# Kernel optimization log

Hardware: AMD Instinct MI355X
Metric: run time of the kernel (lower is better)

The kernel has to match this reference:

```python
import jax, jax.numpy as jnp
import numpy as np

N = 100000      # nodes
E = 1600000     # edges (avg degree 16)
D_IN = 64
D_OUT = 64
EPS = 1e-9


def setup_inputs() -> dict:
    key = jax.random.key(0)
    ks = jax.random.split(key, 12)
    x = jax.random.normal(ks[0], (N, D_IN), dtype=jnp.float32)
    edge_row = jax.random.randint(ks[1], (E,), 0, N, dtype=jnp.int32)
    edge_col = jax.random.randint(ks[2], (E,), 0, N, dtype=jnp.int32)
    # positive normalized adjacency values (~1/degree scale)
    edge_val = jax.random.uniform(ks[3], (E,), dtype=jnp.float32) / 16.0
    lim = float(np.sqrt(6.0 / (D_IN + D_OUT)))  # xavier_uniform
    W0 = jax.random.uniform(ks[4], (D_OUT, D_IN), jnp.float32, -lim, lim)
    W1 = jax.random.uniform(ks[5], (D_OUT, D_IN), jnp.float32, -lim, lim)
    b0 = jnp.zeros((D_OUT,), jnp.float32)
    b1 = jnp.zeros((D_OUT,), jnp.float32)
    scale0 = jnp.ones((D_OUT,), jnp.float32)
    scale1 = jnp.ones((D_OUT,), jnp.float32)
    offset0 = jnp.zeros((D_OUT,), jnp.float32)
    offset1 = jnp.zeros((D_OUT,), jnp.float32)
    return {"x": x, "edge_val": edge_val, "W0": W0, "b0": b0,
            "scale0": scale0, "offset0": offset0, "W1": W1, "b1": b1,
            "scale1": scale1, "offset1": offset1,
            "edge_row": edge_row, "edge_col": edge_col}


def _hop_transform(feat, W, b, scale, offset):
    # Linear (no bias in nn.Linear) + separate bias + ReLU
    h = jax.nn.relu(feat @ W.T + b)                      # [N, D_OUT]
    # custom per-row normalization ('norm' branch)
    mean = jnp.mean(h, axis=1, keepdims=True)
    var = jnp.var(h, axis=1, keepdims=True) + EPS        # unbiased=False
    return (h - mean) * scale * jax.lax.rsqrt(var) + offset


def reference(x, edge_val, W0, b0, scale0, offset0, W1, b1, scale1, offset1,
              edge_row, edge_col):
    # SpMM: out[r] = sum_{e: row[e]==r} val[e] * x[col[e]]
    msgs = edge_val[:, None] * x[edge_col]               # [E, D_IN]
    agg = jax.ops.segment_sum(msgs, edge_row, num_segments=N)
    # order=1: hop-0 uses raw features, hop-1 uses aggregated features
    h0 = _hop_transform(x, W0, b0, scale0, offset0)
    h1 = _hop_transform(agg, W1, b1, scale1, offset1)
    # aggr='mean' -> elementwise sum of partial features
    return h0 + h1
```

## Files before the change

### kernel.cpp

```cpp
#include <hip/hip_runtime.h>

#define NN 100000
#define NE 1600000
#define DD 64
#define P    1563
#define NB   196
#define NBK1 391
#define BCAP 10240
#define PCAP 1536
#define ECAP 1536

__device__ __forceinline__ unsigned short f2bfu(float f) {
    union { float f; unsigned u; } c; c.f = f;
    unsigned lsb = (c.u >> 16) & 1u;
    c.u += 0x7FFFu + lsb;
    return (unsigned short)(c.u >> 16);
}

typedef short v8s __attribute__((ext_vector_type(8)));
typedef float v4f __attribute__((ext_vector_type(4)));

__global__ __launch_bounds__(256) void init_kernel(
    const float* __restrict__ W0, const float* __restrict__ W1,
    int* __restrict__ gbcur,
    unsigned short* __restrict__ wb0, unsigned short* __restrict__ wb1)
{
    int i = blockIdx.x * 256 + threadIdx.x;
    if (i < NB) gbcur[i] = 0;
    if (i < DD * DD) { wb0[i] = f2bfu(W0[i]); wb1[i] = f2bfu(W1[i]); }
}

__global__ __launch_bounds__(256) void bucket_scatter_kernel(
    const int* __restrict__ row, const int* __restrict__ col,
    const float* __restrict__ val, int* __restrict__ gbcur,
    int2* __restrict__ bslab)
{
    __shared__ int hist[NB];
    int b = blockIdx.x, t = threadIdx.x;
    if (t < NB) hist[t] = 0;
    __syncthreads();

    int4 r[4], c[4]; float4 v[4]; bool ok[4];
#pragma unroll
    for (int h = 0; h < 4; ++h) {
        int e = b * 4096 + h * 1024 + t * 4;
        ok[h] = (e + 3 < NE);
        if (ok[h]) {
            r[h] = *(const int4*)(row + e);
            c[h] = *(const int4*)(col + e);
            v[h] = *(const float4*)(val + e);
            atomicAdd(&hist[r[h].x >> 9], 1);
            atomicAdd(&hist[r[h].y >> 9], 1);
            atomicAdd(&hist[r[h].z >> 9], 1);
            atomicAdd(&hist[r[h].w >> 9], 1);
        }
    }
    __syncthreads();
    if (t < NB) {
        int cnt = hist[t];
        hist[t] = cnt ? atomicAdd(&gbcur[t], cnt) : 0;
    }
    __syncthreads();
#pragma unroll
    for (int h = 0; h < 4; ++h) {
        if (ok[h]) {
            int b0_ = r[h].x >> 9, b1_ = r[h].y >> 9;
            int b2_ = r[h].z >> 9, b3_ = r[h].w >> 9;
            int q0 = atomicAdd(&hist[b0_], 1);
            int q1 = atomicAdd(&hist[b1_], 1);
            int q2 = atomicAdd(&hist[b2_], 1);
            int q3 = atomicAdd(&hist[b3_], 1);
            if (q0 < BCAP) bslab[(size_t)b0_ * BCAP + q0] =
                make_int2(c[h].x | ((r[h].x & 511) << 20), __float_as_int(v[h].x));
            if (q1 < BCAP) bslab[(size_t)b1_ * BCAP + q1] =
                make_int2(c[h].y | ((r[h].y & 511) << 20), __float_as_int(v[h].y));
            if (q2 < BCAP) bslab[(size_t)b2_ * BCAP + q2] =
                make_int2(c[h].z | ((r[h].z & 511) << 20), __float_as_int(v[h].z));
            if (q3 < BCAP) bslab[(size_t)b3_ * BCAP + q3] =
                make_int2(c[h].w | ((r[h].w & 511) << 20), __float_as_int(v[h].w));
        }
    }
}

__global__ __launch_bounds__(256) void fine_scatter_kernel(
    const int* __restrict__ gbcur, const int2* __restrict__ bslab,
    int2* __restrict__ fslab, int* __restrict__ fcnt)
{
    __shared__ int cur[8];
    int b = blockIdx.x, t = threadIdx.x;
    int nb = min(gbcur[b], BCAP);
    const int2* bp = bslab + (size_t)b * BCAP;
    if (t < 8) cur[t] = 0;
    __syncthreads();
    for (int i = t; i < nb; i += 256) {
        int2 rc = bp[i];
        int rl = (rc.x >> 20) & 511;
        int lp = rl >> 6;
        int pos = atomicAdd(&cur[lp], 1);
        if (pos < PCAP)
            fslab[(size_t)(b * 8 + lp) * PCAP + pos] =
                make_int2((rc.x & 0x1FFFF) | ((rl & 63) << 20), rc.y);
    }
    __syncthreads();
    if (t < 8) fcnt[b * 8 + t] = min(cur[t], PCAP);
}

__global__ __launch_bounds__(256, 7) void sort_pull_mfma_kernel(
    const float* __restrict__ x, const int* __restrict__ fcnt,
    const int2* __restrict__ fslab,
    const unsigned short* __restrict__ wb0, const unsigned short* __restrict__ wb1,
    const float* __restrict__ b0, const float* __restrict__ s0, const float* __restrict__ o0,
    const float* __restrict__ b1, const float* __restrict__ s1, const float* __restrict__ o1,
    float* __restrict__ out)
{
    __shared__ int2 ebuf[ECAP];
    __shared__ unsigned aggt[4][16][36];
    __shared__ int rcnt[64];
    __shared__ int pscan[64];
    __shared__ int rcur[64];
    __shared__ int pstart[65];

    int p = blockIdx.x, t = threadIdx.x;
    int np = fcnt[p];
    const int2* sp = fslab + (size_t)p * PCAP;

    int2 rec[6]; int nrec = 0;
    if (t < 64) rcnt[t] = 0;
    __syncthreads();
#pragma unroll
    for (int k = 0; k < 6; ++k) {
        int i = t + k * 256;
        if (i < np) {
            rec[k] = sp[i]; ++nrec;
            atomicAdd(&rcnt[(rec[k].x >> 20) & 63], 1);
        }
    }
    __syncthreads();
    if (t < 64) pscan[t] = (rcnt[t] + 7) & ~7;
    __syncthreads();
    for (int off = 1; off < 64; off <<= 1) {
        int u = 0;
        if (t < 64 && t >= off) u = pscan[t - off];
        __syncthreads();
        if (t < 64) pscan[t] += u;
        __syncthreads();
    }
    if (t < 64) pstart[t + 1] = min(pscan[t], ECAP);
    if (t == 0) pstart[0] = 0;
    __syncthreads();
    if (t < 64) {
        rcur[t] = pstart[t];
        int s = min(pstart[t] + rcnt[t], ECAP);
        int e = pstart[t + 1];
        for (int j = s; j < e; ++j) ebuf[j] = make_int2(0, 0);
    }
    __syncthreads();
#pragma unroll
    for (int k = 0; k < 6; ++k) {
        if (k < nrec) {
            int pos = atomicAdd(&rcur[(rec[k].x >> 20) & 63], 1);
            if (pos < ECAP) ebuf[pos] = make_int2(rec[k].x & 0x1FFFF, rec[k].y);
        }
    }
    __syncthreads();

    int lane = t & 63, wv = t >> 6;
    int sub = lane & 15, q = lane >> 4;
    for (int rr = 0; rr < 16; ++rr) {
        int r = wv * 16 + rr;
        int start = pstart[r];
        int cc = (pstart[r + 1] - start) >> 3;
        float4 acc = make_float4(0.f, 0.f, 0.f, 0.f);
        int ch = 0;
        for (; ch + 2 <= cc; ch += 2) {
            int2 r0 = ebuf[start + ch * 8 + q];
            int2 r1 = ebuf[start + ch * 8 + 4 + q];
            int2 r2 = ebuf[start + ch * 8 + 8 + q];
            int2 r3 = ebuf[start + ch * 8 + 12 + q];
            float4 f0 = *(const float4*)(x + (size_t)r0.x * DD + sub * 4);
            float4 f1 = *(const float4*)(x + (size_t)r1.x * DD + sub * 4);
            float4 f2 = *(const float4*)(x + (size_t)r2.x * DD + sub * 4);
            float4 f3 = *(const float4*)(x + (size_t)r3.x * DD + sub * 4);
            float v0 = __int_as_float(r0.y), v1 = __int_as_float(r1.y);
            float v2 = __int_as_float(r2.y), v3 = __int_as_float(r3.y);
            acc.x = fmaf(v0, f0.x, acc.x); acc.y = fmaf(v0, f0.y, acc.y);
            acc.z = fmaf(v0, f0.z, acc.z); acc.w = fmaf(v0, f0.w, acc.w);
            acc.x = fmaf(v1, f1.x, acc.x); acc.y = fmaf(v1, f1.y, acc.y);
            acc.z = fmaf(v1, f1.z, acc.z); acc.w = fmaf(v1, f1.w, acc.w);
            acc.x = fmaf(v2, f2.x, acc.x); acc.y = fmaf(v2, f2.y, acc.y);
            acc.z = fmaf(v2, f2.z, acc.z); acc.w = fmaf(v2, f2.w, acc.w);
            acc.x = fmaf(v3, f3.x, acc.x); acc.y = fmaf(v3, f3.y, acc.y);
            acc.z = fmaf(v3, f3.z, acc.z); acc.w = fmaf(v3, f3.w, acc.w);
        }
        if (ch < cc) {
            int2 r0 = ebuf[start + ch * 8 + q];
            int2 r1 = ebuf[start + ch * 8 + 4 + q];
            float4 f0 = *(const float4*)(x + (size_t)r0.x * DD + sub * 4);
            float4 f1 = *(const float4*)(x + (size_t)r1.x * DD + sub * 4);
            float v0 = __int_as_float(r0.y), v1 = __int_as_float(r1.y);
            acc.x = fmaf(v0, f0.x, acc.x); acc.y = fmaf(v0, f0.y, acc.y);
            acc.z = fmaf(v0, f0.z, acc.z); acc.w = fmaf(v0, f0.w, acc.w);
            acc.x = fmaf(v1, f1.x, acc.x); acc.y = fmaf(v1, f1.y, acc.y);
            acc.z = fmaf(v1, f1.z, acc.z); acc.w = fmaf(v1, f1.w, acc.w);
        }
        acc.x += __shfl_xor(acc.x, 16, 64); acc.y += __shfl_xor(acc.y, 16, 64);
        acc.z += __shfl_xor(acc.z, 16, 64); acc.w += __shfl_xor(acc.w, 16, 64);
        acc.x += __shfl_xor(acc.x, 32, 64); acc.y += __shfl_xor(acc.y, 32, 64);
        acc.z += __shfl_xor(acc.z, 32, 64); acc.w += __shfl_xor(acc.w, 32, 64);
        if (q == 0) {
            uint2 pk;
            pk.x = (unsigned)f2bfu(acc.x) | ((unsigned)f2bfu(acc.y) << 16);
            pk.y = (unsigned)f2bfu(acc.z) | ((unsigned)f2bfu(acc.w) << 16);
            *(uint2*)&aggt[wv][rr][sub * 2] = pk;
        }
    }

    int nb0 = p * 64 + wv * 16;
    if (nb0 >= NN) return;

    v8s ax[2], aa[2];
#pragma unroll
    for (int ks = 0; ks < 2; ++ks) {
        const float* px = x + (size_t)(nb0 + sub) * DD + ks * 32 + q * 8;
        float4 a0 = *(const float4*)px, a1 = *(const float4*)(px + 4);
        v8s w;
        w[0] = (short)f2bfu(a0.x); w[1] = (short)f2bfu(a0.y);
        w[2] = (short)f2bfu(a0.z); w[3] = (short)f2bfu(a0.w);
        w[4] = (short)f2bfu(a1.x); w[5] = (short)f2bfu(a1.y);
        w[6] = (short)f2bfu(a1.z); w[7] = (short)f2bfu(a1.w);
        ax[ks] = w;
        aa[ks] = *(const v8s*)&aggt[wv][sub][ks * 16 + q * 4];
    }

    float h0v[4][4], h1v[4][4];
    float sr0[4] = {0,0,0,0}, sq0[4] = {0,0,0,0};
    float sr1[4] = {0,0,0,0}, sq1[4] = {0,0,0,0};
#pragma unroll
    for (int dt = 0; dt < 4; ++dt) {
        int nidx = dt * 16 + sub;
        float bi0 = b0[nidx], bi1 = b1[nidx];
        v8s w00 = *(const v8s*)(wb0 + nidx * 64 + q * 8);
        v8s w01 = *(const v8s*)(wb0 + nidx * 64 + 32 + q * 8);
        v8s w10 = *(const v8s*)(wb1 + nidx * 64 + q * 8);
        v8s w11 = *(const v8s*)(wb1 + nidx * 64 + 32 + q * 8);
        v4f c0 = (v4f){bi0, bi0, bi0, bi0};
        v4f c1 = (v4f){bi1, bi1, bi1, bi1};
        c0 = __builtin_amdgcn_mfma_f32_16x16x32_bf16(ax[0], w00, c0, 0, 0, 0);
        c0 = __builtin_amdgcn_mfma_f32_16x16x32_bf16(ax[1], w01, c0, 0, 0, 0);
        c1 = __builtin_amdgcn_mfma_f32_16x16x32_bf16(aa[0], w10, c1, 0, 0, 0);
        c1 = __builtin_amdgcn_mfma_f32_16x16x32_bf16(aa[1], w11, c1, 0, 0, 0);
#pragma unroll
        for (int r = 0; r < 4; ++r) {
            float h = fmaxf(c0[r], 0.f); h0v[dt][r] = h; sr0[r] += h; sq0[r] += h * h;
            float g = fmaxf(c1[r], 0.f); h1v[dt][r] = g; sr1[r] += g; sq1[r] += g * g;
        }
    }
#pragma unroll
    for (int off = 1; off < 16; off <<= 1) {
#pragma unroll
        for (int r = 0; r < 4; ++r) {
            sr0[r] += __shfl_xor(sr0[r], off, 64);
            sq0[r] += __shfl_xor(sq0[r], off, 64);
            sr1[r] += __shfl_xor(sr1[r], off, 64);
            sq1[r] += __shfl_xor(sq1[r], off, 64);
        }
    }

    float scl0[4], scl1[4], ofs0[4], ofs1[4];
#pragma unroll
    for (int dt = 0; dt < 4; ++dt) {
        int nidx = dt * 16 + sub;
        scl0[dt] = s0[nidx]; scl1[dt] = s1[nidx];
        ofs0[dt] = o0[nidx]; ofs1[dt] = o1[nidx];
    }

    const float inv = 1.0f / 64.0f;
#pragma unroll
    for (int r = 0; r < 4; ++r) {
        float m0 = sr0[r] * inv;
        float v0 = fmaxf(sq0[r] * inv - m0 * m0, 0.f) + 1e-9f;
        float m1 = sr1[r] * inv;
        float v1 = fmaxf(sq1[r] * inv - m1 * m1, 0.f) + 1e-9f;
        float rs0 = rsqrtf(v0), rs1 = rsqrtf(v1);
        int node = nb0 + q * 4 + r;
#pragma unroll
        for (int dt = 0; dt < 4; ++dt) {
            float rv = (h0v[dt][r] - m0) * scl0[dt] * rs0 + ofs0[dt]
                     + (h1v[dt][r] - m1) * scl1[dt] * rs1 + ofs1[dt];
            out[(size_t)node * DD + dt * 16 + sub] = rv;
        }
    }
}

extern "C" void kernel_launch(void* const* d_in, const int* in_sizes, int n_in,
                              void* d_out, int out_size, void* d_ws, size_t ws_size,
                              hipStream_t stream) {
    const float* x  = (const float*)d_in[0];
    const float* ev = (const float*)d_in[1];
    const float* W0 = (const float*)d_in[2];
    const float* b0 = (const float*)d_in[3];
    const float* s0 = (const float*)d_in[4];
    const float* o0 = (const float*)d_in[5];
    const float* W1 = (const float*)d_in[6];
    const float* b1 = (const float*)d_in[7];
    const float* s1 = (const float*)d_in[8];
    const float* o1 = (const float*)d_in[9];
    const int* row = (const int*)d_in[10];
    const int* col = (const int*)d_in[11];

    char* wsb = (char*)d_ws;
    int*  gbcur = (int*)wsb;
    unsigned short* wb0 = (unsigned short*)(wsb + 1024);
    unsigned short* wb1 = (unsigned short*)(wsb + 9216);
    int*  fcnt  = (int*)(wsb + 17408);
    int2* bslab = (int2*)(wsb + 23808);
    int2* fslab = (int2*)(wsb + 16080128);

    init_kernel<<<16, 256, 0, stream>>>(W0, W1, gbcur, wb0, wb1);
    bucket_scatter_kernel<<<NBK1, 256, 0, stream>>>(row, col, ev, gbcur, bslab);
    fine_scatter_kernel<<<NB, 256, 0, stream>>>(gbcur, bslab, fslab, fcnt);
    sort_pull_mfma_kernel<<<P, 256, 0, stream>>>(
        x, fcnt, fslab, wb0, wb1, b0, s0, o0, b1, s1, o1, (float*)d_out);
}
```

Baseline: 202.2 us.

## Split fine scatter across sub-blocks and interleave two rows in SpMM gather

The fine scatter pass now uses ten blocks per coarse bucket instead of one. Each block runs a local histogram and reserves its output range with global atomics on per-partition cursors, which init_kernel now zeroes. The bucket scatter runs with 512 threads per block, each thread handling fewer edges. The pull kernel processes two destination rows at once with independent accumulators to put more gather loads in flight, and its occupancy hint drops from 7 to 4 blocks, which trades occupancy for more registers per thread.

```diff
diff --git a/kernel.cpp b/kernel.cpp
--- a/kernel.cpp
+++ b/kernel.cpp
@@ -6,6 +6,7 @@
 #define P    1563
 #define NB   196
 #define NBK1 391
+#define NSUB 10
 #define BCAP 10240
 #define PCAP 1536
 #define ECAP 1536
@@ -22,15 +23,16 @@
 
 __global__ __launch_bounds__(256) void init_kernel(
     const float* __restrict__ W0, const float* __restrict__ W1,
-    int* __restrict__ gbcur,
+    int* __restrict__ gbcur, int* __restrict__ fcur,
     unsigned short* __restrict__ wb0, unsigned short* __restrict__ wb1)
 {
     int i = blockIdx.x * 256 + threadIdx.x;
     if (i < NB) gbcur[i] = 0;
+    if (i < NB * 8) fcur[i] = 0;
     if (i < DD * DD) { wb0[i] = f2bfu(W0[i]); wb1[i] = f2bfu(W1[i]); }
 }
 
-__global__ __launch_bounds__(256) void bucket_scatter_kernel(
+__global__ __launch_bounds__(512) void bucket_scatter_kernel(
     const int* __restrict__ row, const int* __restrict__ col,
     const float* __restrict__ val, int* __restrict__ gbcur,
     int2* __restrict__ bslab)
@@ -40,10 +42,10 @@
     if (t < NB) hist[t] = 0;
     __syncthreads();
 
-    int4 r[4], c[4]; float4 v[4]; bool ok[4];
-#pragma unroll
-    for (int h = 0; h < 4; ++h) {
-        int e = b * 4096 + h * 1024 + t * 4;
+    int4 r[2], c[2]; float4 v[2]; bool ok[2];
+#pragma unroll
+    for (int h = 0; h < 2; ++h) {
+        int e = b * 4096 + h * 2048 + t * 4;
         ok[h] = (e + 3 < NE);
         if (ok[h]) {
             r[h] = *(const int4*)(row + e);
@@ -62,7 +64,7 @@
     }
     __syncthreads();
 #pragma unroll
-    for (int h = 0; h < 4; ++h) {
+    for (int h = 0; h < 2; ++h) {
         if (ok[h]) {
             int b0_ = r[h].x >> 9, b1_ = r[h].y >> 9;
             int b2_ = r[h].z >> 9, b3_ = r[h].w >> 9;
@@ -84,28 +86,60 @@
 
 __global__ __launch_bounds__(256) void fine_scatter_kernel(
     const int* __restrict__ gbcur, const int2* __restrict__ bslab,
-    int2* __restrict__ fslab, int* __restrict__ fcnt)
+    int* __restrict__ fcur, int2* __restrict__ fslab)
 {
-    __shared__ int cur[8];
-    int b = blockIdx.x, t = threadIdx.x;
+    __shared__ int cur8[8];
+    int blk = blockIdx.x;
+    int b = blk / NSUB, s = blk - b * NSUB;
     int nb = min(gbcur[b], BCAP);
+    int lo = s * 1024, hi = min(nb, lo + 1024);
+    if (lo >= hi) return;
+    int t = threadIdx.x;
+    if (t < 8) cur8[t] = 0;
+    __syncthreads();
+
     const int2* bp = bslab + (size_t)b * BCAP;
-    if (t < 8) cur[t] = 0;
-    __syncthreads();
-    for (int i = t; i < nb; i += 256) {
-        int2 rc = bp[i];
-        int rl = (rc.x >> 20) & 511;
-        int lp = rl >> 6;
-        int pos = atomicAdd(&cur[lp], 1);
-        if (pos < PCAP)
-            fslab[(size_t)(b * 8 + lp) * PCAP + pos] =
-                make_int2((rc.x & 0x1FFFF) | ((rl & 63) << 20), rc.y);
-    }
-    __syncthreads();
-    if (t < 8) fcnt[b * 8 + t] = min(cur[t], PCAP);
-}
-
-__global__ __launch_bounds__(256, 7) void sort_pull_mfma_kernel(
+    int2 recs[4]; int lps[4]; int nr = 0;
+#pragma unroll
+    for (int k = 0; k < 4; ++k) {
+        int idx = lo + k * 256 + t;
+        if (idx < hi) {
+            recs[nr] = bp[idx];
+            lps[nr] = ((recs[nr].x >> 20) & 511) >> 6;
+            atomicAdd(&cur8[lps[nr]], 1);
+            ++nr;
+        }
+    }
+    __syncthreads();
+    if (t < 8) {
+        int cnt = cur8[t];
+        cur8[t] = cnt ? atomicAdd(&fcur[b * 8 + t], cnt) : 0;
+    }
+    __syncthreads();
+#pragma unroll
+    for (int k = 0; k < 4; ++k) {
+        if (k < nr) {
+            int rl = (recs[k].x >> 20) & 511;
+            int pos = atomicAdd(&cur8[lps[k]], 1);
+            if (pos < PCAP)
+                fslab[(size_t)(b * 8 + lps[k]) * PCAP + pos] =
+                    make_int2((recs[k].x & 0x1FFFF) | ((rl & 63) << 20), recs[k].y);
+        }
+    }
+}
+
+#define GR2(ACC, BASE, CH) { \
+    int2 r0_ = ebuf[(BASE) + (CH) * 8 + q]; \
+    int2 r1_ = ebuf[(BASE) + (CH) * 8 + 4 + q]; \
+    float4 f0_ = *(const float4*)(x + (size_t)r0_.x * DD + sub * 4); \
+    float4 f1_ = *(const float4*)(x + (size_t)r1_.x * DD + sub * 4); \
+    float v0_ = __int_as_float(r0_.y), v1_ = __int_as_float(r1_.y); \
+    ACC.x = fmaf(v0_, f0_.x, ACC.x); ACC.y = fmaf(v0_, f0_.y, ACC.y); \
+    ACC.z = fmaf(v0_, f0_.z, ACC.z); ACC.w = fmaf(v0_, f0_.w, ACC.w); \
+    ACC.x = fmaf(v1_, f1_.x, ACC.x); ACC.y = fmaf(v1_, f1_.y, ACC.y); \
+    ACC.z = fmaf(v1_, f1_.z, ACC.z); ACC.w = fmaf(v1_, f1_.w, ACC.w); }
+
+__global__ __launch_bounds__(256, 4) void sort_pull_mfma_kernel(
     const float* __restrict__ x, const int* __restrict__ fcnt,
     const int2* __restrict__ fslab,
     const unsigned short* __restrict__ wb0, const unsigned short* __restrict__ wb1,
@@ -121,7 +155,7 @@
     __shared__ int pstart[65];
 
     int p = blockIdx.x, t = threadIdx.x;
-    int np = fcnt[p];
+    int np = min(fcnt[p], PCAP);
     const int2* sp = fslab + (size_t)p * PCAP;
 
     int2 rec[6]; int nrec = 0;
@@ -166,52 +200,76 @@
 
     int lane = t & 63, wv = t >> 6;
     int sub = lane & 15, q = lane >> 4;
-    for (int rr = 0; rr < 16; ++rr) {
-        int r = wv * 16 + rr;
-        int start = pstart[r];
-        int cc = (pstart[r + 1] - start) >> 3;
-        float4 acc = make_float4(0.f, 0.f, 0.f, 0.f);
-        int ch = 0;
-        for (; ch + 2 <= cc; ch += 2) {
-            int2 r0 = ebuf[start + ch * 8 + q];
-            int2 r1 = ebuf[start + ch * 8 + 4 + q];
-            int2 r2 = ebuf[start + ch * 8 + 8 + q];
-            int2 r3 = ebuf[start + ch * 8 + 12 + q];
-            float4 f0 = *(const float4*)(x + (size_t)r0.x * DD + sub * 4);
-            float4 f1 = *(const float4*)(x + (size_t)r1.x * DD + sub * 4);
-            float4 f2 = *(const float4*)(x + (size_t)r2.x * DD + sub * 4);
-            float4 f3 = *(const float4*)(x + (size_t)r3.x * DD + sub * 4);
-            float v0 = __int_as_float(r0.y), v1 = __int_as_float(r1.y);
-            float v2 = __int_as_float(r2.y), v3 = __int_as_float(r3.y);
-            acc.x = fmaf(v0, f0.x, acc.x); acc.y = fmaf(v0, f0.y, acc.y);
-            acc.z = fmaf(v0, f0.z, acc.z); acc.w = fmaf(v0, f0.w, acc.w);
-            acc.x = fmaf(v1, f1.x, acc.x); acc.y = fmaf(v1, f1.y, acc.y);
-            acc.z = fmaf(v1, f1.z, acc.z); acc.w = fmaf(v1, f1.w, acc.w);
-            acc.x = fmaf(v2, f2.x, acc.x); acc.y = fmaf(v2, f2.y, acc.y);
-            acc.z = fmaf(v2, f2.z, acc.z); acc.w = fmaf(v2, f2.w, acc.w);
-            acc.x = fmaf(v3, f3.x, acc.x); acc.y = fmaf(v3, f3.y, acc.y);
-            acc.z = fmaf(v3, f3.z, acc.z); acc.w = fmaf(v3, f3.w, acc.w);
-        }
-        if (ch < cc) {
-            int2 r0 = ebuf[start + ch * 8 + q];
-            int2 r1 = ebuf[start + ch * 8 + 4 + q];
-            float4 f0 = *(const float4*)(x + (size_t)r0.x * DD + sub * 4);
-            float4 f1 = *(const float4*)(x + (size_t)r1.x * DD + sub * 4);
-            float v0 = __int_as_float(r0.y), v1 = __int_as_float(r1.y);
-            acc.x = fmaf(v0, f0.x, acc.x); acc.y = fmaf(v0, f0.y, acc.y);
-            acc.z = fmaf(v0, f0.z, acc.z); acc.w = fmaf(v0, f0.w, acc.w);
-            acc.x = fmaf(v1, f1.x, acc.x); acc.y = fmaf(v1, f1.y, acc.y);
-            acc.z = fmaf(v1, f1.z, acc.z); acc.w = fmaf(v1, f1.w, acc.w);
-        }
-        acc.x += __shfl_xor(acc.x, 16, 64); acc.y += __shfl_xor(acc.y, 16, 64);
-        acc.z += __shfl_xor(acc.z, 16, 64); acc.w += __shfl_xor(acc.w, 16, 64);
-        acc.x += __shfl_xor(acc.x, 32, 64); acc.y += __shfl_xor(acc.y, 32, 64);
-        acc.z += __shfl_xor(acc.z, 32, 64); acc.w += __shfl_xor(acc.w, 32, 64);
+    for (int rp = 0; rp < 8; ++rp) {
+        int rA = wv * 16 + rp * 2;
+        int sA = pstart[rA];
+        int sB = pstart[rA + 1];
+        int eB = pstart[rA + 2];
+        int ccA = (sB - sA) >> 3;
+        int ccB = (eB - sB) >> 3;
+        float4 aA = make_float4(0.f, 0.f, 0.f, 0.f);
+        float4 aB = make_float4(0.f, 0.f, 0.f, 0.f);
+        int cA = 0, cB = 0;
+        while (cA + 2 <= ccA && cB + 2 <= ccB) {
+            int2 ra0 = ebuf[sA + cA * 8 + q];
+            int2 ra1 = ebuf[sA + cA * 8 + 4 + q];
+            int2 ra2 = ebuf[sA + cA * 8 + 8 + q];
+            int2 ra3 = ebuf[sA + cA * 8 + 12 + q];
+            int2 rb0 = ebuf[sB + cB * 8 + q];
+            int2 rb1 = ebuf[sB + cB * 8 + 4 + q];
+            int2 rb2 = ebuf[sB + cB * 8 + 8 + q];
+            int2 rb3 = ebuf[sB + cB * 8 + 12 + q];
+            float4 fa0 = *(const float4*)(x + (size_t)ra0.x * DD + sub * 4);
+            float4 fa1 = *(const float4*)(x + (size_t)ra1.x * DD + sub * 4);
+            float4 fa2 = *(const float4*)(x + (size_t)ra2.x * DD + sub * 4);
+            float4 fa3 = *(const float4*)(x + (size_t)ra3.x * DD + sub * 4);
+            float4 fb0 = *(const float4*)(x + (size_t)rb0.x * DD + sub * 4);
+            float4 fb1 = *(const float4*)(x + (size_t)rb1.x * DD + sub * 4);
+            float4 fb2 = *(const float4*)(x + (size_t)rb2.x * DD + sub * 4);
+            float4 fb3 = *(const float4*)(x + (size_t)rb3.x * DD + sub * 4);
+            float va0 = __int_as_float(ra0.y), va1 = __int_as_float(ra1.y);
+            float va2 = __int_as_float(ra2.y), va3 = __int_as_float(ra3.y);
+            float vb0 = __int_as_float(rb0.y), vb1 = __int_as_float(rb1.y);
+            float vb2 = __int_as_float(rb2.y), vb3 = __int_as_float(rb3.y);
+            aA.x = fmaf(va0, fa0.x, aA.x); aA.y = fmaf(va0, fa0.y, aA.y);
+            aA.z = fmaf(va0, fa0.z, aA.z); aA.w = fmaf(va0, fa0.w, aA.w);
+            aA.x = fmaf(va1, fa1.x, aA.x); aA.y = fmaf(va1, fa1.y, aA.y);
+            aA.z = fmaf(va1, fa1.z, aA.z); aA.w = fmaf(va1, fa1.w, aA.w);
+            aA.x = fmaf(va2, fa2.x, aA.x); aA.y = fmaf(va2, fa2.y, aA.y);
+            aA.z = fmaf(va2, fa2.z, aA.z); aA.w = fmaf(va2, fa2.w, aA.w);
+            aA.x = fmaf(va3, fa3.x, aA.x); aA.y = fmaf(va3, fa3.y, aA.y);
+            aA.z = fmaf(va3, fa3.z, aA.z); aA.w = fmaf(va3, fa3.w, aA.w);
+            aB.x = fmaf(vb0, fb0.x, aB.x); aB.y = fmaf(vb0, fb0.y, aB.y);
+            aB.z = fmaf(vb0, fb0.z, aB.z); aB.w = fmaf(vb0, fb0.w, aB.w);
+            aB.x = fmaf(vb1, fb1.x, aB.x); aB.y = fmaf(vb1, fb1.y, aB.y);
+            aB.z = fmaf(vb1, fb1.z, aB.z); aB.w = fmaf(vb1, fb1.w, aB.w);
+            aB.x = fmaf(vb2, fb2.x, aB.x); aB.y = fmaf(vb2, fb2.y, aB.y);
+            aB.z = fmaf(vb2, fb2.z, aB.z); aB.w = fmaf(vb2, fb2.w, aB.w);
+            aB.x = fmaf(vb3, fb3.x, aB.x); aB.y = fmaf(vb3, fb3.y, aB.y);
+            aB.z = fmaf(vb3, fb3.z, aB.z); aB.w = fmaf(vb3, fb3.w, aB.w);
+            cA += 2; cB += 2;
+        }
+        for (; cA + 2 <= ccA; cA += 2) { GR2(aA, sA, cA); GR2(aA, sA, cA + 1); }
+        if (cA < ccA) GR2(aA, sA, cA);
+        for (; cB + 2 <= ccB; cB += 2) { GR2(aB, sB, cB); GR2(aB, sB, cB + 1); }
+        if (cB < ccB) GR2(aB, sB, cB);
+
+        aA.x += __shfl_xor(aA.x, 16, 64); aA.y += __shfl_xor(aA.y, 16, 64);
+        aA.z += __shfl_xor(aA.z, 16, 64); aA.w += __shfl_xor(aA.w, 16, 64);
+        aA.x += __shfl_xor(aA.x, 32, 64); aA.y += __shfl_xor(aA.y, 32, 64);
+        aA.z += __shfl_xor(aA.z, 32, 64); aA.w += __shfl_xor(aA.w, 32, 64);
+        aB.x += __shfl_xor(aB.x, 16, 64); aB.y += __shfl_xor(aB.y, 16, 64);
+        aB.z += __shfl_xor(aB.z, 16, 64); aB.w += __shfl_xor(aB.w, 16, 64);
+        aB.x += __shfl_xor(aB.x, 32, 64); aB.y += __shfl_xor(aB.y, 32, 64);
+        aB.z += __shfl_xor(aB.z, 32, 64); aB.w += __shfl_xor(aB.w, 32, 64);
         if (q == 0) {
-            uint2 pk;
-            pk.x = (unsigned)f2bfu(acc.x) | ((unsigned)f2bfu(acc.y) << 16);
-            pk.y = (unsigned)f2bfu(acc.z) | ((unsigned)f2bfu(acc.w) << 16);
-            *(uint2*)&aggt[wv][rr][sub * 2] = pk;
+            uint2 pkA, pkB;
+            pkA.x = (unsigned)f2bfu(aA.x) | ((unsigned)f2bfu(aA.y) << 16);
+            pkA.y = (unsigned)f2bfu(aA.z) | ((unsigned)f2bfu(aA.w) << 16);
+            pkB.x = (unsigned)f2bfu(aB.x) | ((unsigned)f2bfu(aB.y) << 16);
+            pkB.y = (unsigned)f2bfu(aB.z) | ((unsigned)f2bfu(aB.w) << 16);
+            *(uint2*)&aggt[wv][rp * 2][sub * 2] = pkA;
+            *(uint2*)&aggt[wv][rp * 2 + 1][sub * 2] = pkB;
         }
     }
 
@@ -312,13 +370,13 @@
     int*  gbcur = (int*)wsb;
     unsigned short* wb0 = (unsigned short*)(wsb + 1024);
     unsigned short* wb1 = (unsigned short*)(wsb + 9216);
-    int*  fcnt  = (int*)(wsb + 17408);
+    int*  fcur  = (int*)(wsb + 17408);
     int2* bslab = (int2*)(wsb + 23808);
     int2* fslab = (int2*)(wsb + 16080128);
 
-    init_kernel<<<16, 256, 0, stream>>>(W0, W1, gbcur, wb0, wb1);
-    bucket_scatter_kernel<<<NBK1, 256, 0, stream>>>(row, col, ev, gbcur, bslab);
-    fine_scatter_kernel<<<NB, 256, 0, stream>>>(gbcur, bslab, fslab, fcnt);
+    init_kernel<<<16, 256, 0, stream>>>(W0, W1, gbcur, fcur, wb0, wb1);
+    bucket_scatter_kernel<<<NBK1, 512, 0, stream>>>(row, col, ev, gbcur, bslab);
+    fine_scatter_kernel<<<NB * NSUB, 256, 0, stream>>>(gbcur, bslab, fcur, fslab);
     sort_pull_mfma_kernel<<<P, 256, 0, stream>>>(
-        x, fcnt, fslab, wb0, wb1, b0, s0, o0, b1, s1, o1, (float*)d_out);
-}
+        x, fcur, fslab, wb0, wb1, b0, s0, o0, b1, s1, o1, (float*)d_out);
+}
```

New measurement: 209.6 us. 3.6% more time.

## Sort edges by row in a dedicated kernel and pull from global CSR

Applied to the files above, without the earlier changes.

The pipeline is restructured. Buckets become 256 rows wide, and a new row_sort kernel does the full per-row counting sort in shared memory, writing a compact padded CSR-like array to global memory with a per-node meta word (offset and chunk count). The pull/MFMA kernel no longer sorts in shared memory; it reads edges straight from gsorted, which frees LDS and allows a simpler kernel. The intent is to remove the second scatter pass and the in-kernel sort overhead, at the cost of an extra global write and read of the sorted edges, plus a cap of 16 chunks (128 edges) per row.

```diff
diff --git a/kernel.cpp b/kernel.cpp
--- a/kernel.cpp
+++ b/kernel.cpp
@@ -3,12 +3,12 @@
 #define NN 100000
 #define NE 1600000
 #define DD 64
-#define P    1563
-#define NB   196
+#define NB   391
 #define NBK1 391
-#define BCAP 10240
-#define PCAP 1536
-#define ECAP 1536
+#define BCAP 4608
+#define SCAP 6656
+#define GCAP 2400000
+#define NK3  1563
 
 __device__ __forceinline__ unsigned short f2bfu(float f) {
     union { float f; unsigned u; } c; c.f = f;
@@ -22,15 +22,16 @@
 
 __global__ __launch_bounds__(256) void init_kernel(
     const float* __restrict__ W0, const float* __restrict__ W1,
-    int* __restrict__ gbcur,
+    int* __restrict__ gbcur, int* __restrict__ gtail,
     unsigned short* __restrict__ wb0, unsigned short* __restrict__ wb1)
 {
     int i = blockIdx.x * 256 + threadIdx.x;
     if (i < NB) gbcur[i] = 0;
+    if (i == 0) *gtail = 0;
     if (i < DD * DD) { wb0[i] = f2bfu(W0[i]); wb1[i] = f2bfu(W1[i]); }
 }
 
-__global__ __launch_bounds__(256) void bucket_scatter_kernel(
+__global__ __launch_bounds__(512) void bucket_scatter_kernel(
     const int* __restrict__ row, const int* __restrict__ col,
     const float* __restrict__ val, int* __restrict__ gbcur,
     int2* __restrict__ bslab)
@@ -40,19 +41,19 @@
     if (t < NB) hist[t] = 0;
     __syncthreads();
 
-    int4 r[4], c[4]; float4 v[4]; bool ok[4];
-#pragma unroll
-    for (int h = 0; h < 4; ++h) {
-        int e = b * 4096 + h * 1024 + t * 4;
+    int4 r[2], c[2]; float4 v[2]; bool ok[2];
+#pragma unroll
+    for (int h = 0; h < 2; ++h) {
+        int e = b * 4096 + h * 2048 + t * 4;
         ok[h] = (e + 3 < NE);
         if (ok[h]) {
             r[h] = *(const int4*)(row + e);
             c[h] = *(const int4*)(col + e);
             v[h] = *(const float4*)(val + e);
-            atomicAdd(&hist[r[h].x >> 9], 1);
-            atomicAdd(&hist[r[h].y >> 9], 1);
-            atomicAdd(&hist[r[h].z >> 9], 1);
-            atomicAdd(&hist[r[h].w >> 9], 1);
+            atomicAdd(&hist[r[h].x >> 8], 1);
+            atomicAdd(&hist[r[h].y >> 8], 1);
+            atomicAdd(&hist[r[h].z >> 8], 1);
+            atomicAdd(&hist[r[h].w >> 8], 1);
         }
     }
     __syncthreads();
@@ -62,121 +63,124 @@
     }
     __syncthreads();
 #pragma unroll
-    for (int h = 0; h < 4; ++h) {
+    for (int h = 0; h < 2; ++h) {
         if (ok[h]) {
-            int b0_ = r[h].x >> 9, b1_ = r[h].y >> 9;
-            int b2_ = r[h].z >> 9, b3_ = r[h].w >> 9;
+            int b0_ = r[h].x >> 8, b1_ = r[h].y >> 8;
+            int b2_ = r[h].z >> 8, b3_ = r[h].w >> 8;
             int q0 = atomicAdd(&hist[b0_], 1);
             int q1 = atomicAdd(&hist[b1_], 1);
             int q2 = atomicAdd(&hist[b2_], 1);
             int q3 = atomicAdd(&hist[b3_], 1);
             if (q0 < BCAP) bslab[(size_t)b0_ * BCAP + q0] =
-                make_int2(c[h].x | ((r[h].x & 511) << 20), __float_as_int(v[h].x));
+                make_int2(c[h].x | ((r[h].x & 255) << 17), __float_as_int(v[h].x));
             if (q1 < BCAP) bslab[(size_t)b1_ * BCAP + q1] =
-                make_int2(c[h].y | ((r[h].y & 511) << 20), __float_as_int(v[h].y));
+                make_int2(c[h].y | ((r[h].y & 255) << 17), __float_as_int(v[h].y));
             if (q2 < BCAP) bslab[(size_t)b2_ * BCAP + q2] =
-                make_int2(c[h].z | ((r[h].z & 511) << 20), __float_as_int(v[h].z));
+                make_int2(c[h].z | ((r[h].z & 255) << 17), __float_as_int(v[h].z));
             if (q3 < BCAP) bslab[(size_t)b3_ * BCAP + q3] =
-                make_int2(c[h].w | ((r[h].w & 511) << 20), __float_as_int(v[h].w));
-        }
-    }
-}
-
-__global__ __launch_bounds__(256) void fine_scatter_kernel(
+                make_int2(c[h].w | ((r[h].w & 255) << 17), __float_as_int(v[h].w));
+        }
+    }
+}
+
+__global__ __launch_bounds__(512) void row_sort_kernel(
     const int* __restrict__ gbcur, const int2* __restrict__ bslab,
-    int2* __restrict__ fslab, int* __restrict__ fcnt)
+    int* __restrict__ gtail, int2* __restrict__ gsorted,
+    int* __restrict__ meta)
 {
-    __shared__ int cur[8];
+    __shared__ int2 sorted[SCAP];
+    __shared__ int cnt[256];
+    __shared__ int pscan[256];
+    __shared__ int rcur[256];
+    __shared__ int pstart[257];
+    __shared__ int sh_base8;
+
     int b = blockIdx.x, t = threadIdx.x;
     int nb = min(gbcur[b], BCAP);
     const int2* bp = bslab + (size_t)b * BCAP;
-    if (t < 8) cur[t] = 0;
-    __syncthreads();
-    for (int i = t; i < nb; i += 256) {
-        int2 rc = bp[i];
-        int rl = (rc.x >> 20) & 511;
-        int lp = rl >> 6;
-        int pos = atomicAdd(&cur[lp], 1);
-        if (pos < PCAP)
-            fslab[(size_t)(b * 8 + lp) * PCAP + pos] =
-                make_int2((rc.x & 0x1FFFF) | ((rl & 63) << 20), rc.y);
-    }
-    __syncthreads();
-    if (t < 8) fcnt[b * 8 + t] = min(cur[t], PCAP);
-}
-
-__global__ __launch_bounds__(256, 7) void sort_pull_mfma_kernel(
-    const float* __restrict__ x, const int* __restrict__ fcnt,
-    const int2* __restrict__ fslab,
+
+    int2 rec[9]; int rl[9]; int nr = 0;
+    if (t < 256) cnt[t] = 0;
+    __syncthreads();
+#pragma unroll
+    for (int k = 0; k < 9; ++k) {
+        int i = t + k * 512;
+        if (i < nb) {
+            rec[nr] = bp[i];
+            rl[nr] = (rec[nr].x >> 17) & 255;
+            atomicAdd(&cnt[rl[nr]], 1);
+            ++nr;
+        }
+    }
+    __syncthreads();
+    if (t < 256) pscan[t] = (cnt[t] + 7) & ~7;
+    __syncthreads();
+    for (int off = 1; off < 256; off <<= 1) {
+        int u = 0;
+        if (t < 256 && t >= off) u = pscan[t - off];
+        __syncthreads();
+        if (t < 256) pscan[t] += u;
+        __syncthreads();
+    }
+    if (t < 256) pstart[t + 1] = pscan[t];
+    if (t == 0) {
+        pstart[0] = 0;
+        sh_base8 = atomicAdd(gtail, pscan[255] >> 3);
+    }
+    __syncthreads();
+    int base8 = sh_base8;
+    if (t < 256) {
+        rcur[t] = pstart[t];
+        int s = pstart[t] + cnt[t], e = pstart[t + 1];
+        for (int j = s; j < e; ++j) sorted[j] = make_int2(0, 0);
+        int n = b * 256 + t;
+        int cc = min((e - pstart[t]) >> 3, 16);
+        int s8 = base8 + (pstart[t] >> 3);
+        meta[n] = (s8 << 5) | cc;
+    }
+    __syncthreads();
+#pragma unroll
+    for (int k = 0; k < 9; ++k) {
+        if (k < nr) {
+            int pos = atomicAdd(&rcur[rl[k]], 1);
+            if (pos < SCAP) sorted[pos] = make_int2(rec[k].x & 0x1FFFF, rec[k].y);
+        }
+    }
+    __syncthreads();
+    int tp = pscan[255];
+    int gb = base8 * 8;
+    for (int i = t; i < tp; i += 512) {
+        int gi = gb + i;
+        if (gi < GCAP) gsorted[gi] = sorted[i];
+    }
+}
+
+__global__ __launch_bounds__(256, 4) void pull_mfma_kernel(
+    const float* __restrict__ x, const int* __restrict__ meta,
+    const int2* __restrict__ gsorted,
     const unsigned short* __restrict__ wb0, const unsigned short* __restrict__ wb1,
     const float* __restrict__ b0, const float* __restrict__ s0, const float* __restrict__ o0,
     const float* __restrict__ b1, const float* __restrict__ s1, const float* __restrict__ o1,
     float* __restrict__ out)
 {
-    __shared__ int2 ebuf[ECAP];
     __shared__ unsigned aggt[4][16][36];
-    __shared__ int rcnt[64];
-    __shared__ int pscan[64];
-    __shared__ int rcur[64];
-    __shared__ int pstart[65];
-
-    int p = blockIdx.x, t = threadIdx.x;
-    int np = fcnt[p];
-    const int2* sp = fslab + (size_t)p * PCAP;
-
-    int2 rec[6]; int nrec = 0;
-    if (t < 64) rcnt[t] = 0;
-    __syncthreads();
-#pragma unroll
-    for (int k = 0; k < 6; ++k) {
-        int i = t + k * 256;
-        if (i < np) {
-            rec[k] = sp[i]; ++nrec;
-            atomicAdd(&rcnt[(rec[k].x >> 20) & 63], 1);
-        }
-    }
-    __syncthreads();
-    if (t < 64) pscan[t] = (rcnt[t] + 7) & ~7;
-    __syncthreads();
-    for (int off = 1; off < 64; off <<= 1) {
-        int u = 0;
-        if (t < 64 && t >= off) u = pscan[t - off];
-        __syncthreads();
-        if (t < 64) pscan[t] += u;
-        __syncthreads();
-    }
-    if (t < 64) pstart[t + 1] = min(pscan[t], ECAP);
-    if (t == 0) pstart[0] = 0;
-    __syncthreads();
-    if (t < 64) {
-        rcur[t] = pstart[t];
-        int s = min(pstart[t] + rcnt[t], ECAP);
-        int e = pstart[t + 1];
-        for (int j = s; j < e; ++j) ebuf[j] = make_int2(0, 0);
-    }
-    __syncthreads();
-#pragma unroll
-    for (int k = 0; k < 6; ++k) {
-        if (k < nrec) {
-            int pos = atomicAdd(&rcur[(rec[k].x >> 20) & 63], 1);
-            if (pos < ECAP) ebuf[pos] = make_int2(rec[k].x & 0x1FFFF, rec[k].y);
-        }
-    }
-    __syncthreads();
-
-    int lane = t & 63, wv = t >> 6;
+
+    int t = threadIdx.x, lane = t & 63, wv = t >> 6;
     int sub = lane & 15, q = lane >> 4;
+    int nb0 = blockIdx.x * 64 + wv * 16;
+    if (nb0 >= NN) return;
+
     for (int rr = 0; rr < 16; ++rr) {
-        int r = wv * 16 + rr;
-        int start = pstart[r];
-        int cc = (pstart[r + 1] - start) >> 3;
+        int mt = meta[nb0 + rr];
+        int cc = mt & 31;
+        const int2* rp = gsorted + ((size_t)(mt >> 5) << 3);
         float4 acc = make_float4(0.f, 0.f, 0.f, 0.f);
         int ch = 0;
         for (; ch + 2 <= cc; ch += 2) {
-            int2 r0 = ebuf[start + ch * 8 + q];
-            int2 r1 = ebuf[start + ch * 8 + 4 + q];
-            int2 r2 = ebuf[start + ch * 8 + 8 + q];
-            int2 r3 = ebuf[start + ch * 8 + 12 + q];
+            int2 r0 = rp[ch * 8 + q];
+            int2 r1 = rp[ch * 8 + 4 + q];
+            int2 r2 = rp[ch * 8 + 8 + q];
+            int2 r3 = rp[ch * 8 + 12 + q];
             float4 f0 = *(const float4*)(x + (size_t)r0.x * DD + sub * 4);
             float4 f1 = *(const float4*)(x + (size_t)r1.x * DD + sub * 4);
             float4 f2 = *(const float4*)(x + (size_t)r2.x * DD + sub * 4);
@@ -193,8 +197,8 @@
             acc.z = fmaf(v3, f3.z, acc.z); acc.w = fmaf(v3, f3.w, acc.w);
         }
         if (ch < cc) {
-            int2 r0 = ebuf[start + ch * 8 + q];
-            int2 r1 = ebuf[start + ch * 8 + 4 + q];
+            int2 r0 = rp[ch * 8 + q];
+            int2 r1 = rp[ch * 8 + 4 + q];
             float4 f0 = *(const float4*)(x + (size_t)r0.x * DD + sub * 4);
             float4 f1 = *(const float4*)(x + (size_t)r1.x * DD + sub * 4);
             float v0 = __int_as_float(r0.y), v1 = __int_as_float(r1.y);
@@ -214,9 +218,6 @@
             *(uint2*)&aggt[wv][rr][sub * 2] = pk;
         }
     }
-
-    int nb0 = p * 64 + wv * 16;
-    if (nb0 >= NN) return;
 
     v8s ax[2], aa[2];
 #pragma unroll
@@ -310,15 +311,16 @@
 
     char* wsb = (char*)d_ws;
     int*  gbcur = (int*)wsb;
-    unsigned short* wb0 = (unsigned short*)(wsb + 1024);
-    unsigned short* wb1 = (unsigned short*)(wsb + 9216);
-    int*  fcnt  = (int*)(wsb + 17408);
-    int2* bslab = (int2*)(wsb + 23808);
-    int2* fslab = (int2*)(wsb + 16080128);
-
-    init_kernel<<<16, 256, 0, stream>>>(W0, W1, gbcur, wb0, wb1);
-    bucket_scatter_kernel<<<NBK1, 256, 0, stream>>>(row, col, ev, gbcur, bslab);
-    fine_scatter_kernel<<<NB, 256, 0, stream>>>(gbcur, bslab, fslab, fcnt);
-    sort_pull_mfma_kernel<<<P, 256, 0, stream>>>(
-        x, fcnt, fslab, wb0, wb1, b0, s0, o0, b1, s1, o1, (float*)d_out);
-}
+    int*  gtail = (int*)(wsb + 1600);
+    unsigned short* wb0 = (unsigned short*)(wsb + 1664);
+    unsigned short* wb1 = (unsigned short*)(wsb + 9856);
+    int*  meta  = (int*)(wsb + 18176);
+    int2* bslab = (int2*)(wsb + 418816);
+    int2* gsorted = (int2*)(wsb + 14832640);
+
+    init_kernel<<<16, 256, 0, stream>>>(W0, W1, gbcur, gtail, wb0, wb1);
+    bucket_scatter_kernel<<<NBK1, 512, 0, stream>>>(row, col, ev, gbcur, bslab);
+    row_sort_kernel<<<NB, 512, 0, stream>>>(gbcur, bslab, gtail, gsorted, meta);
+    pull_mfma_kernel<<<NK3, 256, 0, stream>>>(
+        x, meta, gsorted, wb0, wb1, b0, s0, o0, b1, s1, o1, (float*)d_out);
+}
```

Result: slower. 221.5 us (+9.5%).
